# Performance work log

Hardware: AMD Instinct MI355X
Metric: run time of the kernel (lower is better)

## Reference

```python
import jax, jax.numpy as jnp
import numpy as np

B = 512
AUDIO_H, VIDEO_H, TEXT_H = 64, 64, 128
POST_DIM = 128
FUSION_DIM = (TEXT_H + 1) * (VIDEO_H + 1) * (AUDIO_H + 1)  # 129*65*65 = 545025


def setup_inputs() -> dict:
    key = jax.random.key(0)
    ks = jax.random.split(key, 9)
    s1 = 1.0 / np.sqrt(FUSION_DIM)
    s2 = 1.0 / np.sqrt(POST_DIM)
    return {
        "audio_h": jax.random.normal(ks[0], (B, AUDIO_H), jnp.float32),
        "video_h": jax.random.normal(ks[1], (B, VIDEO_H), jnp.float32),
        "text_h": jax.random.normal(ks[2], (B, TEXT_H), jnp.float32),
        "W1": jax.random.uniform(ks[3], (FUSION_DIM, POST_DIM), jnp.float32, -s1, s1),
        "b1": jax.random.uniform(ks[4], (POST_DIM,), jnp.float32, -s1, s1),
        "W2": jax.random.uniform(ks[5], (POST_DIM, POST_DIM), jnp.float32, -s2, s2),
        "b2": jax.random.uniform(ks[6], (POST_DIM,), jnp.float32, -s2, s2),
        "W3": jax.random.uniform(ks[7], (POST_DIM, 1), jnp.float32, -s2, s2),
        "b3": jax.random.uniform(ks[8], (1,), jnp.float32, -s2, s2),
    }


def reference(audio_h, video_h, text_h, W1, b1, W2, b2, W3, b3):
    b = audio_h.shape[0]
    ones = jnp.ones((b, 1), audio_h.dtype)
    a1 = jnp.concatenate([ones, audio_h], axis=1)  # [B, A+1]
    v1 = jnp.concatenate([ones, video_h], axis=1)  # [B, V+1]
    t1 = jnp.concatenate([ones, text_h], axis=1)   # [B, T+1]
    # trilinear outer product: [B, T+1, V+1, A+1]
    fusion = jnp.einsum('bi,bj,bk->bijk', t1, v1, a1)
    flat = fusion.reshape(b, -1)  # [B, FUSION_DIM]
    # post-fusion MLP (dropout probs = 0 -> identity at inference)
    y1 = jax.nn.relu(flat @ W1 + b1)
    y2 = jax.nn.relu(y1 @ W2 + b2)
    y3 = jax.nn.sigmoid(y2 @ W3 + b3)
    # affine map to [-3, 3]: output_range=6, output_shift=-3
    return y3 * 6.0 - 3.0
```

## Files before the change

### kernel.cpp

```cpp
#include <hip/hip_runtime.h>
#include <hip/hip_bf16.h>
#include <math.h>

#define POST 128
#define NI 129
#define NJK 4225
#define NTOT 16512
#define KBLKS 134
#define MBLKS 32
#define KSTEPS32 134
#define KHALF 67
#define PANEL_CLAMP 2163184u

typedef __attribute__((ext_vector_type(8))) short bf16x8;
typedef __attribute__((ext_vector_type(4))) float f32x4;
typedef __attribute__((ext_vector_type(4))) unsigned int u32x4;

__device__ __forceinline__ unsigned short f2bf(float f){
    unsigned u = __builtin_bit_cast(unsigned, f);
    unsigned r = (u + 0x7FFFu + ((u >> 16) & 1u)) >> 16;
    return (unsigned short)r;
}
__device__ __forceinline__ unsigned pack2(float a, float b){
    return (unsigned)f2bf(a) | ((unsigned)f2bf(b) << 16);
}
__device__ __forceinline__ unsigned cvtpk(float lo, float hi){
    unsigned r;
    asm("v_cvt_pk_bf16_f32 %0, %1, %2" : "=v"(r) : "v"(lo), "v"(hi));
    return r;
}

__device__ __forceinline__ void gload16(const void* g, void* l){
    __builtin_amdgcn_global_load_lds(
        (const __attribute__((address_space(1))) unsigned int*)g,
        (__attribute__((address_space(3))) unsigned int*)l, 16, 0, 0);
}

__global__ void build_af(const float* __restrict__ audio,
                         const float* __restrict__ video,
                         uint4* __restrict__ af)
{
    int gid = blockIdx.x * 256 + threadIdx.x;
    if (gid >= KBLKS * MBLKS * 64) return;
    int lane = gid & 63;
    int mblk = (gid >> 6) & 31;
    int kblk = gid >> 11;
    int m  = mblk * 16 + (lane & 15);
    int k0 = kblk * 32 + (lane >> 4) * 8;
    float vals[8];
#pragma unroll
    for (int j = 0; j < 8; ++j){
        int k = k0 + j;
        float p = 0.f;
        if (k < NJK){
            int jj = k / 65;
            int kk = k - jj * 65;
            float a = (kk == 0) ? 1.f : audio[m * 64 + kk - 1];
            float v = (jj == 0) ? 1.f : video[m * 64 + jj - 1];
            p = a * v;
        }
        vals[j] = p;
    }
    uint4 o;
    o.x = pack2(vals[0], vals[1]);
    o.y = pack2(vals[2], vals[3]);
    o.z = pack2(vals[4], vals[5]);
    o.w = pack2(vals[6], vals[7]);
    af[gid] = o;
}

__global__ __launch_bounds__(256, 2) void fusion_gemm(
    const float* __restrict__ W1,
    const uint4* __restrict__ af,
    float* __restrict__ Z0,
    float* __restrict__ Z1)
{
    __shared__ __align__(16) char lds[81920];

    int orig = blockIdx.x;
    int xcd  = orig & 7;
    int base = (xcd < 4) ? xcd * 65 : 260 + (xcd - 4) * 64;
    int w    = base + (orig >> 3);
    int nt  = w >> 2;
    int sub = w & 3;
    int mt  = sub & 1;
    int kb  = sub >> 1;

    int it0 = kb * KHALF;

    int t    = threadIdx.x;
    int lane = t & 63;
    int wv   = t >> 6;

    f32x4 acc[4][8] = {};

    const char* wpanel = (const char*)(W1 + (size_t)nt * (NJK * 128));
    const char* afb    = (const char*)af;

    int n_c = t & 127;
    int kg  = t >> 7;

#define STAGE(ks_, pb_)                                                         \
    do {                                                                        \
        char* dstA_ = lds + (pb_) * 16384;                                      \
        char* dstB_ = lds + 32768 + (pb_) * 16384;                              \
        _Pragma("unroll")                                                       \
        for (int i_ = 0; i_ < 8; ++i_){                                         \
            int c_ = wv * 8 + i_;                                               \
            if (c_ < 16){                                                       \
                const char* s_ = afb + (size_t)(ks_) * 32768                    \
                               + (size_t)(mt * 16 + c_) * 1024 + lane * 16;     \
                gload16(s_, dstA_ + c_ * 1024);                                 \
            } else {                                                            \
                int cb_ = c_ - 16;                                              \
                unsigned bo_ = (unsigned)(ks_) * 16384u                         \
                             + (unsigned)cb_ * 1024u + (unsigned)lane * 16u;    \
                if (bo_ > PANEL_CLAMP) bo_ = PANEL_CLAMP;        \
                gload16(wpanel + bo_, dstB_ + cb_ * 1024);                      \
            }                                                                   \
        }                                                                       \
    } while (0)

    STAGE(it0, 0);

    for (int it = 0; it < KHALF; ++it){
        int ks = it0 + it;
        int p  = it & 1;

        asm volatile("s_waitcnt vmcnt(0)" ::: "memory");
        __builtin_amdgcn_s_barrier();

        if (it + 1 < KHALF)
            STAGE(ks + 1, p ^ 1);

        {
            const char* rawp = lds + 32768 + p * 16384;
            char* fragp      = lds + 65536 + p * 8192;
            float v[16];
#pragma unroll
            for (int j = 0; j < 16; ++j)
                v[j] = *(const float*)(rawp + (kg * 16 + j) * 512 + n_c * 4);
            u32x4 u0, u1;
            u0.x = cvtpk(v[0],  v[1]);  u0.y = cvtpk(v[2],  v[3]);
            u0.z = cvtpk(v[4],  v[5]);  u0.w = cvtpk(v[6],  v[7]);
            u1.x = cvtpk(v[8],  v[9]);  u1.y = cvtpk(v[10], v[11]);
            u1.z = cvtpk(v[12], v[13]); u1.w = cvtpk(v[14], v[15]);
            int swz = ((n_c >> 1) & 3) << 4;
            *(u32x4*)(fragp + ((n_c * 64 + kg * 32     ) ^ swz)) = u0;
            *(u32x4*)(fragp + ((n_c * 64 + kg * 32 + 16) ^ swz)) = u1;
        }
        asm volatile("s_waitcnt lgkmcnt(0)" ::: "memory");
        __builtin_amdgcn_sched_barrier(0);
        __builtin_amdgcn_s_barrier();

        {
            const char* sa    = lds + p * 16384;
            const char* fragp = lds + 65536 + p * 8192;
            bf16x8 a[4];
#pragma unroll
            for (int f = 0; f < 4; ++f)
                a[f] = *(const bf16x8*)(sa + (wv * 4 + f) * 1024 + lane * 16);
#pragma unroll
            for (int g = 0; g < 8; ++g){
                int n = g * 16 + (lane & 15);
                int byte = (n * 64 + (lane >> 4) * 16) ^ (((n >> 1) & 3) << 4);
                bf16x8 bg = *(const bf16x8*)(fragp + byte);
#pragma unroll
                for (int f = 0; f < 4; ++f)
                    acc[f][g] = __builtin_amdgcn_mfma_f32_16x16x32_bf16(a[f], bg, acc[f][g], 0, 0, 0);
            }
        }
    }

    float* Zp = kb ? Z1 : Z0;
    int row0 = mt * 256 + wv * 64 + (lane >> 4) * 4;
    int col0 = nt * 128 + (lane & 15);
#pragma unroll
    for (int f = 0; f < 4; ++f)
#pragma unroll
        for (int g = 0; g < 8; ++g)
#pragma unroll
            for (int r = 0; r < 4; ++r)
                Zp[(size_t)(row0 + f * 16 + r) * NTOT + col0 + g * 16] = acc[f][g][r];
}

__global__ void tail_mlp(const float* __restrict__ Z0,
                         const float* __restrict__ Z1,
                         const float* __restrict__ text,
                         const float* __restrict__ b1,
                         const float* __restrict__ W2,
                         const float* __restrict__ b2,
                         const float* __restrict__ W3,
                         const float* __restrict__ b3,
                         float* __restrict__ out)
{
    int b   = blockIdx.x;
    int tid = threadIdx.x;
    __shared__ float t1s[NI];
    __shared__ float y1s[POST];
    __shared__ float red[2];

    t1s[tid + 1] = text[b * 128 + tid];
    if (tid == 0) t1s[0] = 1.f;
    __syncthreads();

    const float* z0 = Z0 + (size_t)b * NTOT;
    const float* z1 = Z1 + (size_t)b * NTOT;
    float acc = 0.f;
    for (int i = 0; i < NI; ++i)
        acc = fmaf(t1s[i], z0[i * 128 + tid] + z1[i * 128 + tid], acc);
    acc += b1[tid];
    float y1 = fmaxf(acc, 0.f);
    y1s[tid] = y1;
    __syncthreads();

    float a2 = b2[tid];
    for (int q = 0; q < 128; ++q)
        a2 = fmaf(y1s[q], W2[q * 128 + tid], a2);
    float y2 = fmaxf(a2, 0.f);

    float part = y2 * W3[tid];
#pragma unroll
    for (int off = 32; off > 0; off >>= 1)
        part += __shfl_down(part, off);
    if ((tid & 63) == 0) red[tid >> 6] = part;
    __syncthreads();
    if (tid == 0){
        float z = red[0] + red[1] + b3[0];
        out[b] = 6.f / (1.f + expf(-z)) - 3.f;
    }
}

extern "C" void kernel_launch(void* const* d_in, const int* in_sizes, int n_in,
                              void* d_out, int out_size, void* d_ws, size_t ws_size,
                              hipStream_t stream)
{
    const float* audio = (const float*)d_in[0];
    const float* video = (const float*)d_in[1];
    const float* text  = (const float*)d_in[2];
    const float* W1    = (const float*)d_in[3];
    const float* b1    = (const float*)d_in[4];
    const float* W2    = (const float*)d_in[5];
    const float* b2    = (const float*)d_in[6];
    const float* W3    = (const float*)d_in[7];
    const float* b3    = (const float*)d_in[8];
    float* out = (float*)d_out;

    char* ws = (char*)d_ws;
    uint4* af = (uint4*)ws;
    float* Z0 = (float*)(ws + (8u  << 20));
    float* Z1 = (float*)(ws + (48u << 20));

    int af_granules = KBLKS * MBLKS * 64;
    build_af<<<(af_granules + 255) / 256, 256, 0, stream>>>(audio, video, af);
    fusion_gemm<<<516, 256, 0, stream>>>(W1, af, Z0, Z1);
    tail_mlp<<<512, 128, 0, stream>>>(Z0, Z1, text, b1, W2, b2, W3, b3, out);
}
```

Measured before the change: 189.1 us.

## Shrink GEMM M tile, load A fragments directly to registers, raise occupancy

The fusion GEMM block tile changes from 256 rows to 128 rows, with four blocks per N tile instead of two, which doubles the grid to 1032 blocks. The 2x2 wave layout gives each wave a 64x64 output. A-operand fragments now come straight from global memory into registers instead of being staged through LDS. LDS shrinks to 32KB with a single raw W1 staging buffer, and launch bounds allow four blocks per CU to raise occupancy. The cost is that each W1 panel is now read by twice as many blocks, roughly doubling W1 bandwidth. The reordered barrier and prefetch with single buffering may also expose more latency.

```diff
diff --git a/kernel.cpp b/kernel.cpp
--- a/kernel.cpp
+++ b/kernel.cpp
@@ -8,7 +8,6 @@
 #define NTOT 16512
 #define KBLKS 134
 #define MBLKS 32
-#define KSTEPS32 134
 #define KHALF 67
 #define PANEL_CLAMP 2163184u
 
@@ -69,77 +68,71 @@
     af[gid] = o;
 }
 
-__global__ __launch_bounds__(256, 2) void fusion_gemm(
+__global__ __launch_bounds__(256, 4) void fusion_gemm(
     const float* __restrict__ W1,
     const uint4* __restrict__ af,
     float* __restrict__ Z0,
     float* __restrict__ Z1)
 {
-    __shared__ __align__(16) char lds[81920];
+    __shared__ __align__(16) char lds[32768];
 
     int orig = blockIdx.x;
     int xcd  = orig & 7;
-    int base = (xcd < 4) ? xcd * 65 : 260 + (xcd - 4) * 64;
-    int w    = base + (orig >> 3);
-    int nt  = w >> 2;
-    int sub = w & 3;
-    int mt  = sub & 1;
-    int kb  = sub >> 1;
-
-    int it0 = kb * KHALF;
+    int w    = xcd * 129 + (orig >> 3);
+    int nt  = w >> 3;
+    int sub = w & 7;
+    int mt  = sub & 3;
+    int kb  = sub >> 2;
 
     int t    = threadIdx.x;
     int lane = t & 63;
     int wv   = t >> 6;
-
-    f32x4 acc[4][8] = {};
+    int wm   = wv >> 1, wn = wv & 1;
+
+    f32x4 acc[4][4] = {};
 
     const char* wpanel = (const char*)(W1 + (size_t)nt * (NJK * 128));
-    const char* afb    = (const char*)af;
 
     int n_c = t & 127;
     int kg  = t >> 7;
 
-#define STAGE(ks_, pb_)                                                         \
+    int ks0 = kb * KHALF;
+
+#define STAGE(ks_)                                                              \
     do {                                                                        \
-        char* dstA_ = lds + (pb_) * 16384;                                      \
-        char* dstB_ = lds + 32768 + (pb_) * 16384;                              \
         _Pragma("unroll")                                                       \
-        for (int i_ = 0; i_ < 8; ++i_){                                         \
-            int c_ = wv * 8 + i_;                                               \
-            if (c_ < 16){                                                       \
-                const char* s_ = afb + (size_t)(ks_) * 32768                    \
-                               + (size_t)(mt * 16 + c_) * 1024 + lane * 16;     \
-                gload16(s_, dstA_ + c_ * 1024);                                 \
-            } else {                                                            \
-                int cb_ = c_ - 16;                                              \
-                unsigned bo_ = (unsigned)(ks_) * 16384u                         \
-                             + (unsigned)cb_ * 1024u + (unsigned)lane * 16u;    \
-                if (bo_ > PANEL_CLAMP) bo_ = PANEL_CLAMP;        \
-                gload16(wpanel + bo_, dstB_ + cb_ * 1024);                      \
-            }                                                                   \
+        for (int i_ = 0; i_ < 4; ++i_){                                         \
+            int c_ = wv * 4 + i_;                                               \
+            unsigned bo_ = (unsigned)(ks_) * 16384u                             \
+                         + (unsigned)c_ * 1024u + (unsigned)lane * 16u;         \
+            if (bo_ > PANEL_CLAMP) bo_ = PANEL_CLAMP;            \
+            gload16(wpanel + bo_, lds + c_ * 1024);                             \
         }                                                                       \
     } while (0)
 
-    STAGE(it0, 0);
+    STAGE(ks0);
 
     for (int it = 0; it < KHALF; ++it){
-        int ks = it0 + it;
+        int ks = ks0 + it;
         int p  = it & 1;
 
-        asm volatile("s_waitcnt vmcnt(0)" ::: "memory");
+        const uint4* abase = af + ((size_t)ks * 32 + mt * 8 + wm * 4) * 64 + lane;
+        uint4 vA0 = abase[0];
+        uint4 vA1 = abase[64];
+        uint4 vA2 = abase[128];
+        uint4 vA3 = abase[192];
+        __builtin_amdgcn_sched_barrier(0);
+
+        asm volatile("s_waitcnt vmcnt(4)" ::: "memory");
+        __builtin_amdgcn_sched_barrier(0);
         __builtin_amdgcn_s_barrier();
 
-        if (it + 1 < KHALF)
-            STAGE(ks + 1, p ^ 1);
-
         {
-            const char* rawp = lds + 32768 + p * 16384;
-            char* fragp      = lds + 65536 + p * 8192;
+            char* fragp = lds + 16384 + p * 8192;
             float v[16];
 #pragma unroll
             for (int j = 0; j < 16; ++j)
-                v[j] = *(const float*)(rawp + (kg * 16 + j) * 512 + n_c * 4);
+                v[j] = *(const float*)(lds + (kg * 16 + j) * 512 + n_c * 4);
             u32x4 u0, u1;
             u0.x = cvtpk(v[0],  v[1]);  u0.y = cvtpk(v[2],  v[3]);
             u0.z = cvtpk(v[4],  v[5]);  u0.w = cvtpk(v[6],  v[7]);
@@ -153,32 +146,40 @@
         __builtin_amdgcn_sched_barrier(0);
         __builtin_amdgcn_s_barrier();
 
+        if (it + 1 < KHALF)
+            STAGE(ks + 1);
+        __builtin_amdgcn_sched_barrier(0);
+
         {
-            const char* sa    = lds + p * 16384;
-            const char* fragp = lds + 65536 + p * 8192;
-            bf16x8 a[4];
-#pragma unroll
-            for (int f = 0; f < 4; ++f)
-                a[f] = *(const bf16x8*)(sa + (wv * 4 + f) * 1024 + lane * 16);
-#pragma unroll
-            for (int g = 0; g < 8; ++g){
-                int n = g * 16 + (lane & 15);
+            const char* fragp = lds + 16384 + p * 8192;
+            bf16x8 b[4];
+#pragma unroll
+            for (int g = 0; g < 4; ++g){
+                int n = wn * 64 + g * 16 + (lane & 15);
                 int byte = (n * 64 + (lane >> 4) * 16) ^ (((n >> 1) & 3) << 4);
-                bf16x8 bg = *(const bf16x8*)(fragp + byte);
-#pragma unroll
-                for (int f = 0; f < 4; ++f)
-                    acc[f][g] = __builtin_amdgcn_mfma_f32_16x16x32_bf16(a[f], bg, acc[f][g], 0, 0, 0);
+                b[g] = *(const bf16x8*)(fragp + byte);
+            }
+            bf16x8 a0 = __builtin_bit_cast(bf16x8, vA0);
+            bf16x8 a1 = __builtin_bit_cast(bf16x8, vA1);
+            bf16x8 a2 = __builtin_bit_cast(bf16x8, vA2);
+            bf16x8 a3 = __builtin_bit_cast(bf16x8, vA3);
+#pragma unroll
+            for (int g = 0; g < 4; ++g){
+                acc[0][g] = __builtin_amdgcn_mfma_f32_16x16x32_bf16(a0, b[g], acc[0][g], 0, 0, 0);
+                acc[1][g] = __builtin_amdgcn_mfma_f32_16x16x32_bf16(a1, b[g], acc[1][g], 0, 0, 0);
+                acc[2][g] = __builtin_amdgcn_mfma_f32_16x16x32_bf16(a2, b[g], acc[2][g], 0, 0, 0);
+                acc[3][g] = __builtin_amdgcn_mfma_f32_16x16x32_bf16(a3, b[g], acc[3][g], 0, 0, 0);
             }
         }
     }
 
     float* Zp = kb ? Z1 : Z0;
-    int row0 = mt * 256 + wv * 64 + (lane >> 4) * 4;
-    int col0 = nt * 128 + (lane & 15);
+    int row0 = mt * 128 + wm * 64 + (lane >> 4) * 4;
+    int col0 = nt * 128 + wn * 64 + (lane & 15);
 #pragma unroll
     for (int f = 0; f < 4; ++f)
 #pragma unroll
-        for (int g = 0; g < 8; ++g)
+        for (int g = 0; g < 4; ++g)
 #pragma unroll
             for (int r = 0; r < 4; ++r)
                 Zp[(size_t)(row0 + f * 16 + r) * NTOT + col0 + g * 16] = acc[f][g][r];
@@ -253,6 +254,6 @@
 
     int af_granules = KBLKS * MBLKS * 64;
     build_af<<<(af_granules + 255) / 256, 256, 0, stream>>>(audio, video, af);
-    fusion_gemm<<<516, 256, 0, stream>>>(W1, af, Z0, Z1);
+    fusion_gemm<<<1032, 256, 0, stream>>>(W1, af, Z0, Z1);
     tail_mlp<<<512, 128, 0, stream>>>(Z0, Z1, text, b1, W2, b2, W3, b3, out);
 }
```

After: 190.8 us. Within noise of the previous version (+0.9%).
